# Kernel optimization log

Hardware: AMD Instinct MI355X
Metric: run time of the kernel (lower is better)

Reference implementation:

```python
import jax, jax.numpy as jnp
import numpy as np

N_NODES = 100000
NEG_SLOPE = 0.2  # PyG GATConv default LeakyReLU slope


def gat_conv(x, W, att_src, att_dst, bias, edge_index, num_nodes, concat):
    """PyG-style GATConv with default add_self_loops=True.
    x: [N, Fin], W: [Fin, H*C], att_src/att_dst: [H, C], bias: [H*C] or [C].
    """
    H, C = att_src.shape
    h = (x @ W).reshape(num_nodes, H, C)              # [N, H, C]
    # append self-loops (PyG default)
    loops = jnp.arange(num_nodes, dtype=edge_index.dtype)
    src = jnp.concatenate([edge_index[0], loops])     # [E+N]
    dst = jnp.concatenate([edge_index[1], loops])
    # per-node attention logits, then per-edge score
    a_src = jnp.sum(h * att_src[None], axis=-1)       # [N, H]
    a_dst = jnp.sum(h * att_dst[None], axis=-1)       # [N, H]
    e = jax.nn.leaky_relu(a_src[src] + a_dst[dst], NEG_SLOPE)  # [E+N, H]
    # softmax over incoming edges of each destination node
    m = jax.ops.segment_max(e, dst, num_segments=num_nodes)    # [N, H]
    e = jnp.exp(e - m[dst])
    denom = jax.ops.segment_sum(e, dst, num_segments=num_nodes)
    alpha = e / denom[dst]                                      # [E+N, H]
    # scatter-aggregate weighted source features
    msg = h[src] * alpha[..., None]                             # [E+N, H, C]
    out = jax.ops.segment_sum(msg, dst, num_segments=num_nodes)  # [N, H, C]
    if concat:
        out = out.reshape(num_nodes, H * C)
    else:
        out = out.mean(axis=1)
    return out + bias


def setup_inputs() -> dict:
    key = jax.random.key(0)
    ks = jax.random.split(key, 12)
    N, E = N_NODES, 1600000
    Fin, Ch, Hh, Cout = 128, 64, 2, 64

    def glorot(k, shape):
        fan = shape[0] + shape[-1]
        return jax.random.uniform(k, shape, jnp.float32, -1.0, 1.0) * np.sqrt(6.0 / fan)

    x = jax.random.normal(ks[0], (N, Fin), jnp.float32)
    edge_index = jax.random.randint(ks[1], (2, E), 0, N, jnp.int32)
    W1 = glorot(ks[2], (Fin, Hh * Ch))
    att_src1 = glorot(ks[3], (Hh, Ch))
    att_dst1 = glorot(ks[4], (Hh, Ch))
    b1 = jnp.zeros((Hh * Ch,), jnp.float32)
    W2 = glorot(ks[5], (Hh * Ch, Cout))
    att_src2 = glorot(ks[6], (1, Cout))
    att_dst2 = glorot(ks[7], (1, Cout))
    b2 = jnp.zeros((Cout,), jnp.float32)
    return {"x": x, "edge_index": edge_index,
            "W1": W1, "att_src1": att_src1, "att_dst1": att_dst1, "b1": b1,
            "W2": W2, "att_src2": att_src2, "att_dst2": att_dst2, "b2": b2}


def reference(x, edge_index, W1, att_src1, att_dst1, b1, W2, att_src2, att_dst2, b2):
    h = gat_conv(x, W1, att_src1, att_dst1, b1, edge_index, N_NODES, concat=True)
    h = jax.nn.elu(h)
    out = gat_conv(h, W2, att_src2, att_dst2, b2, edge_index, N_NODES, concat=True)
    return out
```

## Files before the change

kernel.cpp:

```cpp
#include <hip/hip_runtime.h>
#include <hip/hip_bf16.h>
#include <cstdint>
#include <cstddef>

static constexpr int FIN = 128;
static constexpr int HC1 = 128;
static constexpr int EPB = 4096;

typedef __attribute__((ext_vector_type(8))) short short8;
typedef __attribute__((ext_vector_type(4))) float f32x4;

__device__ __forceinline__ float bf2f(unsigned int u) { return __uint_as_float(u << 16); }
__device__ __forceinline__ unsigned short f2bf(float f) {
  unsigned int u = __float_as_uint(f);
  return (unsigned short)((u + 0x7fff + ((u >> 16) & 1)) >> 16);
}
__device__ __forceinline__ float lrelu02(float x) { return x > 0.f ? x : 0.2f * x; }
__device__ __forceinline__ int rl_i(int v, int l) { return __builtin_amdgcn_readlane(v, l); }
__device__ __forceinline__ unsigned int q8b(float x, float inv) {
  float q = fminf(fmaxf(x * inv, -127.f), 127.f);
  return (unsigned int)((int)rintf(q) + 128) & 255u;
}
#define NEG_INF __int_as_float(0xff800000)

__global__ __launch_bounds__(256) void bucket_hist(const int* __restrict__ dst,
                                                   int* __restrict__ bhist, int E, int NB) {
  __shared__ int lh[512];
  int t = threadIdx.x;
  lh[t] = 0; lh[t + 256] = 0;
  __syncthreads();
  int e0 = blockIdx.x * EPB;
  #pragma unroll
  for (int i = 0; i < EPB / 256; i++) {
    int e = e0 + i * 256 + t;
    if (e < E) atomicAdd(&lh[dst[e] >> 8], 1);
  }
  __syncthreads();
  for (int x = t; x < NB; x += 256) {
    int c = lh[x];
    if (c > 0) atomicAdd(&bhist[x], c);
  }
}

__global__ __launch_bounds__(512) void scan_buckets(const int* __restrict__ bhist,
                                                    int* __restrict__ boffs, int n) {
  __shared__ int sh[512];
  int t = threadIdx.x;
  int v = (t < n) ? bhist[t] : 0;
  sh[t] = v; __syncthreads();
  for (int d = 1; d < 512; d <<= 1) {
    int w = (t >= d) ? sh[t - d] : 0;
    __syncthreads();
    sh[t] += w;
    __syncthreads();
  }
  if (t <= n) boffs[t] = sh[t] - v;
}

__global__ __launch_bounds__(256) void bucket_scatter(const int* __restrict__ src,
                                                      const int* __restrict__ dst,
                                                      const int* __restrict__ boffs,
                                                      int* __restrict__ gcur,
                                                      unsigned int* __restrict__ sorted,
                                                      int E, int NB) {
  __shared__ int lh[512];
  int t = threadIdx.x;
  lh[t] = 0; lh[t + 256] = 0;
  __syncthreads();
  int e0 = blockIdx.x * EPB;
  #pragma unroll
  for (int i = 0; i < EPB / 256; i++) {
    int e = e0 + i * 256 + t;
    if (e < E) atomicAdd(&lh[dst[e] >> 8], 1);
  }
  __syncthreads();
  for (int x = t; x < NB; x += 256) {
    int c = lh[x];
    lh[x] = (c > 0) ? (boffs[x] + atomicAdd(&gcur[x], c)) : 0;
  }
  __syncthreads();
  #pragma unroll
  for (int i = 0; i < EPB / 256; i++) {
    int e = e0 + i * 256 + t;
    if (e < E) {
      int d = dst[e];
      int pos = atomicAdd(&lh[d >> 8], 1);
      sorted[pos] = ((unsigned int)src[e] << 8) | (unsigned int)(d & 255);
    }
  }
}

__global__ __launch_bounds__(256) void bucket_place_fused(const unsigned int* __restrict__ sorted,
                                                          const int* __restrict__ boffs,
                                                          int* __restrict__ offs,
                                                          int* __restrict__ ssrc,
                                                          int N, int E) {
  __shared__ int cnt[256];
  __shared__ int pref[256];
  int b = blockIdx.x, t = threadIdx.x;
  cnt[t] = 0;
  __syncthreads();
  int beg = boffs[b], end = boffs[b + 1];
  for (int p = beg + t; p < end; p += 256)
    atomicAdd(&cnt[sorted[p] & 255u], 1);
  __syncthreads();
  int v = cnt[t];
  pref[t] = v; __syncthreads();
  for (int d = 1; d < 256; d <<= 1) {
    int w = (t >= d) ? pref[t - d] : 0;
    __syncthreads();
    pref[t] += w;
    __syncthreads();
  }
  int excl = pref[t] - v;
  int node = b * 256 + t;
  if (node < N) offs[node] = beg + excl;
  if (b == 0 && t == 0) offs[N] = E;
  cnt[t] = beg + excl;
  __syncthreads();
  for (int p = beg + t; p < end; p += 256) {
    unsigned int pk = sorted[p];
    int dl = pk & 255u;
    int r = atomicAdd(&cnt[dl], 1);
    ssrc[r] = (int)(pk >> 8);
  }
}

template <int COLS, bool AF32>
__global__ __launch_bounds__(256) void gemm_mfma(const void* __restrict__ Av,
                                                 const float* __restrict__ Wv,
                                                 const float* __restrict__ att_s,
                                                 const float* __restrict__ att_d,
                                                 unsigned char* __restrict__ Cq,
                                                 float* __restrict__ scl,
                                                 float* __restrict__ asrc,
                                                 float* __restrict__ adst,
                                                 int nrows) {
  constexpr int NT = COLS / 16;
  constexpr int H = COLS / 64;
  __shared__ unsigned short WT[COLS][136];
  __shared__ __align__(16) unsigned char pack[4][16 * COLS];

  const int tid = threadIdx.x;
  constexpr int NPC = COLS / 4;
  for (int idx = tid; idx < 128 * NPC; idx += 256) {
    int k = idx / NPC;
    int n0 = (idx - k * NPC) * 4;
    float4 wv = *(const float4*)(Wv + (size_t)k * COLS + n0);
    WT[n0 + 0][k] = f2bf(wv.x);
    WT[n0 + 1][k] = f2bf(wv.y);
    WT[n0 + 2][k] = f2bf(wv.z);
    WT[n0 + 3][k] = f2bf(wv.w);
  }

  const int w = tid >> 6, lane = tid & 63;
  const int quad = lane >> 4, cl = lane & 15;
  const int rbase = blockIdx.x * 128 + w * 32;

  float asv[NT], adv[NT];
  #pragma unroll
  for (int ct = 0; ct < NT; ct++) {
    asv[ct] = att_s[ct * 16 + cl];
    adv[ct] = att_d[ct * 16 + cl];
  }
  __syncthreads();

  f32x4 acc[2][NT];
  #pragma unroll
  for (int rt = 0; rt < 2; rt++)
    #pragma unroll
    for (int ct = 0; ct < NT; ct++) acc[rt][ct] = (f32x4){0.f, 0.f, 0.f, 0.f};

  #pragma unroll
  for (int kc = 0; kc < 4; kc++) {
    const int k0 = kc * 32 + quad * 8;
    short8 a[2];
    #pragma unroll
    for (int rt = 0; rt < 2; rt++) {
      int row = rbase + rt * 16 + cl;
      row = min(row, nrows - 1);
      if constexpr (AF32) {
        const float* ap = (const float*)Av + (size_t)row * 128 + k0;
        float4 f0 = *(const float4*)ap;
        float4 f1 = *(const float4*)(ap + 4);
        short8 t;
        t[0] = (short)f2bf(f0.x); t[1] = (short)f2bf(f0.y);
        t[2] = (short)f2bf(f0.z); t[3] = (short)f2bf(f0.w);
        t[4] = (short)f2bf(f1.x); t[5] = (short)f2bf(f1.y);
        t[6] = (short)f2bf(f1.z); t[7] = (short)f2bf(f1.w);
        a[rt] = t;
      } else {
        a[rt] = *(const short8*)((const unsigned short*)Av + (size_t)row * 128 + k0);
      }
    }
    #pragma unroll
    for (int ct = 0; ct < NT; ct++) {
      short8 b = *(const short8*)&WT[ct * 16 + cl][k0];
      #pragma unroll
      for (int rt = 0; rt < 2; rt++)
        acc[rt][ct] = __builtin_amdgcn_mfma_f32_16x16x32_bf16(a[rt], b, acc[rt][ct], 0, 0, 0);
    }
  }

  #pragma unroll
  for (int rt = 0; rt < 2; rt++) {
    #pragma unroll
    for (int r = 0; r < 4; r++) {
      int grow = rbase + rt * 16 + quad * 4 + r;
      float s0 = 0.f, s1 = 0.f, d0 = 0.f, d1 = 0.f;
      float mx = 0.f;
      #pragma unroll
      for (int ct = 0; ct < NT; ct++) {
        float av = acc[rt][ct][r];
        mx = fmaxf(mx, fabsf(av));
        if (H == 2 && ct >= NT / 2) {
          s1 = fmaf(av, asv[ct], s1);
          d1 = fmaf(av, adv[ct], d1);
        } else {
          s0 = fmaf(av, asv[ct], s0);
          d0 = fmaf(av, adv[ct], d0);
        }
      }
      #pragma unroll
      for (int dd = 8; dd >= 1; dd >>= 1) {
        mx = fmaxf(mx, __shfl_xor(mx, dd));
        s0 += __shfl_xor(s0, dd);
        d0 += __shfl_xor(d0, dd);
        if (H == 2) {
          s1 += __shfl_xor(s1, dd);
          d1 += __shfl_xor(d1, dd);
        }
      }
      float inv = mx > 0.f ? 127.f / mx : 0.f;
      if (cl == 0 && grow < nrows) {
        scl[grow] = mx * (1.f / 127.f);
        if (H == 2) {
          ((float2*)asrc)[grow] = make_float2(s0, s1);
          ((float2*)adst)[grow] = make_float2(d0, d1);
        } else {
          asrc[grow] = s0;
          adst[grow] = d0;
        }
      }
      #pragma unroll
      for (int ct = 0; ct < NT; ct++)
        pack[w][(quad * 4 + r) * COLS + ct * 16 + cl] =
            (unsigned char)q8b(acc[rt][ct][r], inv);
    }
    __syncthreads();
    if constexpr (COLS == 128) {
      #pragma unroll
      for (int i = 0; i < 2; i++) {
        int off = i * 1024 + lane * 16;
        uint4 v = *(const uint4*)&pack[w][off];
        int grow = rbase + rt * 16 + (off >> 7);
        if (grow < nrows)
          *(uint4*)(Cq + (size_t)grow * 128 + (off & 127)) = v;
      }
    } else {
      int off = lane * 16;
      uint4 v = *(const uint4*)&pack[w][off];
      int grow = rbase + rt * 16 + (off >> 6);
      if (grow < nrows)
        *(uint4*)(Cq + (size_t)grow * 64 + (off & 63)) = v;
    }
    __syncthreads();
  }
}

template <int H, bool ELU_OUT, bool F32OUT>
__global__ __launch_bounds__(256) void agg_gather(const void* __restrict__ hq,
                                                  const float* __restrict__ scl,
                                                  const float* __restrict__ asrc,
                                                  const float* __restrict__ adst,
                                                  const int* __restrict__ offs,
                                                  const int* __restrict__ ssrc,
                                                  const float* __restrict__ bias,
                                                  void* __restrict__ outv, int n) {
  __shared__ float pshare[4][64];
  __shared__ int vshare[4][64];
  const int tid = threadIdx.x;
  const int wid = tid >> 6;
  int node = (int)((blockIdx.x * (unsigned)blockDim.x + tid) >> 6);
  int lane = tid & 63;
  if (node >= n) return;
  const int hd = lane >> 5;
  const int beg = offs[node], end = offs[node + 1];
  const unsigned short* hq16 = (const unsigned short*)hq;
  const unsigned char* hqb = (const unsigned char*)hq;

  float adh, m, acc0, acc1, d;
  float SPF = 0.f;
  const float s_self = scl[node];
  if constexpr (H == 2) {
    float2 adv = ((const float2*)adst)[node];
    float2 asv = ((const float2*)asrc)[node];
    adh = hd ? adv.y : adv.x;
    m = lrelu02((hd ? asv.y : asv.x) + adh);
    unsigned int v = hq16[((size_t)node << 6) + lane];
    acc0 = s_self * ((float)(v & 255u) - 128.f);
    acc1 = s_self * ((float)((v >> 8) & 255u) - 128.f);
  } else {
    adh = adst[node];
    m = lrelu02(asrc[node] + adh);
    if (hd == 0) {
      unsigned int v = hq16[((size_t)node << 5) + lane];
      acc0 = s_self * ((float)(v & 255u) - 128.f);
      acc1 = s_self * ((float)((v >> 8) & 255u) - 128.f);
    } else {
      acc0 = 0.f; acc1 = 0.f;
    }
  }
  d = 1.f;

  constexpr int CH = (H == 2) ? 32 : 64;
  const int lvoff = (lane & 31) * 2;
  for (int pos = beg; pos < end; pos += CH) {
    const int len = min(CH, end - pos);
    int li = (H == 2) ? (lane & 31) : lane;
    bool valid = li < len;
    int s_l = valid ? ssrc[pos + li] : 0;
    float scl_l = valid ? scl[s_l] : 0.f;
    float e_l;
    if constexpr (H == 2) {
      float a = asrc[(s_l << 1) + hd];
      e_l = valid ? lrelu02(a + adh) : NEG_INF;
    } else {
      float a = asrc[s_l];
      e_l = valid ? lrelu02(a + adh) : NEG_INF;
    }
    float mc = e_l;
    #pragma unroll
    for (int dlt = CH >> 1; dlt >= 1; dlt >>= 1) mc = fmaxf(mc, __shfl_xor(mc, dlt));
    float m_new = fmaxf(m, mc);
    float f = __expf(m - m_new);
    float p_l = __expf(e_l - m_new);
    float sc = p_l;
    #pragma unroll
    for (int dlt = CH >> 1; dlt >= 1; dlt >>= 1) sc += __shfl_xor(sc, dlt);
    d = d * f + sc;
    acc0 *= f; acc1 *= f;
    m = m_new;
    p_l *= scl_l;

    pshare[wid][lane] = p_l;
    float spf = p_l;
    if constexpr (H == 2) {
      #pragma unroll
      for (int dlt = 16; dlt >= 1; dlt >>= 1) spf += __shfl_xor(spf, dlt);
    } else {
      vshare[wid][lane] = s_l << 6;
      #pragma unroll
      for (int dlt = 32; dlt >= 1; dlt >>= 1) spf += __shfl_xor(spf, dlt);
    }
    SPF = SPF * f + spf;

    if constexpr (H == 2) {
      const int ng = (len + 7) >> 3;
      for (int g = 0; g < ng; g++) {
        const int jb = g * 8;
        unsigned short v[8];
        #pragma unroll
        for (int k = 0; k < 8; k++) {
          int s = rl_i(s_l, jb + k);
          v[k] = hq16[((size_t)(unsigned)s << 6) + lane];
        }
        float pv[8];
        #pragma unroll
        for (int k = 0; k < 8; k++) pv[k] = pshare[wid][hd * 32 + jb + k];
        #pragma unroll
        for (int k = 0; k < 8; k++) {
          unsigned int w = v[k];
          acc0 = fmaf(pv[k], (float)(w & 255u), acc0);
          acc1 = fmaf(pv[k], (float)((w >> 8) & 255u), acc1);
        }
      }
    } else {
      const int npair = (len + 1) >> 1;
      const int ng = (npair + 7) >> 3;
      for (int g = 0; g < ng; g++) {
        const int jb = g * 16;
        unsigned short v[8];
        #pragma unroll
        for (int k = 0; k < 8; k++) {
          int voff = vshare[wid][jb + 2 * k + hd];
          v[k] = *(const unsigned short*)(hqb + (unsigned)voff + lvoff);
        }
        float pv[8];
        #pragma unroll
        for (int k = 0; k < 8; k++) pv[k] = pshare[wid][jb + 2 * k + hd];
        #pragma unroll
        for (int k = 0; k < 8; k++) {
          unsigned int w = v[k];
          acc0 = fmaf(pv[k], (float)(w & 255u), acc0);
          acc1 = fmaf(pv[k], (float)((w >> 8) & 255u), acc1);
        }
      }
    }
  }

  if constexpr (H == 1) {
    acc0 += __shfl_xor(acc0, 32);
    acc1 += __shfl_xor(acc1, 32);
  }
  acc0 = fmaf(-128.f, SPF, acc0);
  acc1 = fmaf(-128.f, SPF, acc1);

  const float inv = 1.f / d;
  if constexpr (H == 2) {
    float2 bv = ((const float2*)bias)[lane];
    float v0 = acc0 * inv + bv.x;
    float v1 = acc1 * inv + bv.y;
    if (ELU_OUT) {
      v0 = v0 > 0.f ? v0 : (__expf(v0) - 1.f);
      v1 = v1 > 0.f ? v1 : (__expf(v1) - 1.f);
    }
    if constexpr (F32OUT) {
      ((float2*)outv)[(size_t)node * 64 + lane] = make_float2(v0, v1);
    } else {
      unsigned int pk = (unsigned int)f2bf(v0) | ((unsigned int)f2bf(v1) << 16);
      ((unsigned int*)outv)[(size_t)node * 64 + lane] = pk;
    }
  } else {
    if (hd == 0) {
      float2 bv = ((const float2*)bias)[lane];
      float v0 = acc0 * inv + bv.x;
      float v1 = acc1 * inv + bv.y;
      if (ELU_OUT) {
        v0 = v0 > 0.f ? v0 : (__expf(v0) - 1.f);
        v1 = v1 > 0.f ? v1 : (__expf(v1) - 1.f);
      }
      if constexpr (F32OUT) {
        ((float2*)outv)[(size_t)node * 32 + lane] = make_float2(v0, v1);
      } else {
        unsigned int pk = (unsigned int)f2bf(v0) | ((unsigned int)f2bf(v1) << 16);
        ((unsigned int*)outv)[(size_t)node * 32 + lane] = pk;
      }
    }
  }
}

extern "C" void kernel_launch(void* const* d_in, const int* in_sizes, int n_in,
                              void* d_out, int out_size, void* d_ws, size_t ws_size,
                              hipStream_t stream) {
  const int N = in_sizes[0] / FIN;
  const int E = in_sizes[1] / 2;

  const void*  x   = d_in[0];
  const int*   ei  = (const int*)d_in[1];
  const float* W1  = (const float*)d_in[2];
  const float* as1 = (const float*)d_in[3];
  const float* ad1 = (const float*)d_in[4];
  const float* b1  = (const float*)d_in[5];
  const float* W2  = (const float*)d_in[6];
  const float* as2 = (const float*)d_in[7];
  const float* ad2 = (const float*)d_in[8];
  const float* b2  = (const float*)d_in[9];

  const int* e_src = ei;
  const int* e_dst = ei + E;

  char* p = (char*)d_ws;
  auto carve = [&](size_t bytes) {
    char* q = p;
    p += (bytes + 255) & ~(size_t)255;
    return (void*)q;
  };
  unsigned char* h1q = (unsigned char*)carve((size_t)N * 128);
  float* scl1        = (float*)carve((size_t)N * 4);
  unsigned char* h2q = (unsigned char*)carve((size_t)N * 64);
  float* scl2        = (float*)carve((size_t)N * 4);
  unsigned short* buf2 = (unsigned short*)carve((size_t)N * HC1 * 2);
  float* asrc1 = (float*)carve((size_t)N * 2 * 4);
  float* adst1 = (float*)carve((size_t)N * 2 * 4);
  float* asrc2 = (float*)carve((size_t)N * 4);
  float* adst2 = (float*)carve((size_t)N * 4);
  int* offs    = (int*)carve((size_t)(N + 1) * 4);
  int* bhist   = (int*)carve((size_t)2 * 512 * 4);
  int* gcur    = bhist + 512;
  int* boffs   = (int*)carve(513 * 4);
  unsigned int* sorted = (unsigned int*)carve((size_t)E * 4);
  int* ssrc    = (int*)carve((size_t)E * 4);

  const int NB = (N + 255) >> 8;
  const int sgrid = (E + EPB - 1) / EPB;
  const int wgrid = (int)(((size_t)N * 64 + 255) / 256);
  const int ggrid = (N + 127) / 128;

  hipMemsetAsync(bhist, 0, (size_t)2 * 512 * 4, stream);
  bucket_hist<<<sgrid, 256, 0, stream>>>(e_dst, bhist, E, NB);
  scan_buckets<<<1, 512, 0, stream>>>(bhist, boffs, NB);
  bucket_scatter<<<sgrid, 256, 0, stream>>>(e_src, e_dst, boffs, gcur, sorted, E, NB);
  bucket_place_fused<<<NB, 256, 0, stream>>>(sorted, boffs, offs, ssrc, N, E);

  gemm_mfma<128, true><<<ggrid, 256, 0, stream>>>(x, W1, as1, ad1, h1q, scl1,
                                                  asrc1, adst1, N);
  agg_gather<2, true, false><<<wgrid, 256, 0, stream>>>(h1q, scl1, asrc1, adst1, offs, ssrc,
                                                        b1, buf2, N);

  gemm_mfma<64, false><<<ggrid, 256, 0, stream>>>(buf2, W2, as2, ad2, h2q, scl2,
                                                  asrc2, adst2, N);
  agg_gather<1, false, true><<<wgrid, 256, 0, stream>>>(h2q, scl2, asrc2, adst2, offs, ssrc,
                                                        b2, d_out, N);
}
```

Measured before the change: 311.1 us.

## Replace online softmax with global-max upper bound for attention normalization

The GEMM kernels now compute a global maximum of the source attention logits per head with atomicMax on order-preserving float keys. The aggregation kernel uses lrelu(max_src + a_dst) as a fixed per-node upper bound on the softmax shift. This removes the per-chunk wave max/sum reductions and the rescaling of accumulators from the online softmax, deferring the sums to one final reduction. The bound is valid because LeakyReLU is monotone, but a loose bound can cause exp underflow for nodes whose logits sit far below the global maximum.

```diff
diff --git a/kernel.cpp b/kernel.cpp
--- a/kernel.cpp
+++ b/kernel.cpp
@@ -20,6 +20,13 @@
 __device__ __forceinline__ unsigned int q8b(float x, float inv) {
   float q = fminf(fmaxf(x * inv, -127.f), 127.f);
   return (unsigned int)((int)rintf(q) + 128) & 255u;
+}
+__device__ __forceinline__ unsigned int fkey(float f) {
+  unsigned int u = __float_as_uint(f);
+  return (int)u < 0 ? ~u : (u | 0x80000000u);
+}
+__device__ __forceinline__ float fdec(unsigned int k) {
+  return __uint_as_float((int)k < 0 ? (k & 0x7fffffffu) : ~k);
 }
 #define NEG_INF __int_as_float(0xff800000)
 
@@ -135,6 +142,7 @@
                                                  float* __restrict__ scl,
                                                  float* __restrict__ asrc,
                                                  float* __restrict__ adst,
+                                                 unsigned int* __restrict__ gmax,
                                                  int nrows) {
   constexpr int NT = COLS / 16;
   constexpr int H = COLS / 64;
@@ -202,6 +210,7 @@
     }
   }
 
+  float lm0 = NEG_INF, lm1 = NEG_INF;
   #pragma unroll
   for (int rt = 0; rt < 2; rt++) {
     #pragma unroll
@@ -231,6 +240,8 @@
           d1 += __shfl_xor(d1, dd);
         }
       }
+      lm0 = fmaxf(lm0, s0);
+      if (H == 2) lm1 = fmaxf(lm1, s1);
       float inv = mx > 0.f ? 127.f / mx : 0.f;
       if (cl == 0 && grow < nrows) {
         scl[grow] = mx * (1.f / 127.f);
@@ -266,6 +277,17 @@
     }
     __syncthreads();
   }
+
+  lm0 = fmaxf(lm0, __shfl_xor(lm0, 16));
+  lm0 = fmaxf(lm0, __shfl_xor(lm0, 32));
+  if (H == 2) {
+    lm1 = fmaxf(lm1, __shfl_xor(lm1, 16));
+    lm1 = fmaxf(lm1, __shfl_xor(lm1, 32));
+  }
+  if (lane == 0) {
+    atomicMax(gmax + 0, fkey(lm0));
+    if (H == 2) atomicMax(gmax + 1, fkey(lm1));
+  }
 }
 
 template <int H, bool ELU_OUT, bool F32OUT>
@@ -273,6 +295,7 @@
                                                   const float* __restrict__ scl,
                                                   const float* __restrict__ asrc,
                                                   const float* __restrict__ adst,
+                                                  const unsigned int* __restrict__ gmax,
                                                   const int* __restrict__ offs,
                                                   const int* __restrict__ ssrc,
                                                   const float* __restrict__ bias,
@@ -289,29 +312,35 @@
   const unsigned short* hq16 = (const unsigned short*)hq;
   const unsigned char* hqb = (const unsigned char*)hq;
 
-  float adh, m, acc0, acc1, d;
-  float SPF = 0.f;
+  float adh, B, p_self, acc0, acc1;
   const float s_self = scl[node];
   if constexpr (H == 2) {
     float2 adv = ((const float2*)adst)[node];
     float2 asv = ((const float2*)asrc)[node];
     adh = hd ? adv.y : adv.x;
-    m = lrelu02((hd ? asv.y : asv.x) + adh);
+    float es = lrelu02((hd ? asv.y : asv.x) + adh);
+    B = lrelu02(fdec(gmax[hd]) + adh);
+    p_self = __expf(es - B);
     unsigned int v = hq16[((size_t)node << 6) + lane];
-    acc0 = s_self * ((float)(v & 255u) - 128.f);
-    acc1 = s_self * ((float)((v >> 8) & 255u) - 128.f);
+    float ps = p_self * s_self;
+    acc0 = ps * ((float)(v & 255u) - 128.f);
+    acc1 = ps * ((float)((v >> 8) & 255u) - 128.f);
   } else {
     adh = adst[node];
-    m = lrelu02(asrc[node] + adh);
+    float es = lrelu02(asrc[node] + adh);
+    B = lrelu02(fdec(gmax[0]) + adh);
+    p_self = __expf(es - B);
     if (hd == 0) {
       unsigned int v = hq16[((size_t)node << 5) + lane];
-      acc0 = s_self * ((float)(v & 255u) - 128.f);
-      acc1 = s_self * ((float)((v >> 8) & 255u) - 128.f);
+      float ps = p_self * s_self;
+      acc0 = ps * ((float)(v & 255u) - 128.f);
+      acc1 = ps * ((float)((v >> 8) & 255u) - 128.f);
     } else {
       acc0 = 0.f; acc1 = 0.f;
     }
   }
-  d = 1.f;
+  float dacc = 0.f;
+  float SPF = 0.f;
 
   constexpr int CH = (H == 2) ? 32 : 64;
   const int lvoff = (lane & 31) * 2;
@@ -321,39 +350,16 @@
     bool valid = li < len;
     int s_l = valid ? ssrc[pos + li] : 0;
     float scl_l = valid ? scl[s_l] : 0.f;
-    float e_l;
-    if constexpr (H == 2) {
-      float a = asrc[(s_l << 1) + hd];
-      e_l = valid ? lrelu02(a + adh) : NEG_INF;
-    } else {
-      float a = asrc[s_l];
-      e_l = valid ? lrelu02(a + adh) : NEG_INF;
-    }
-    float mc = e_l;
-    #pragma unroll
-    for (int dlt = CH >> 1; dlt >= 1; dlt >>= 1) mc = fmaxf(mc, __shfl_xor(mc, dlt));
-    float m_new = fmaxf(m, mc);
-    float f = __expf(m - m_new);
-    float p_l = __expf(e_l - m_new);
-    float sc = p_l;
-    #pragma unroll
-    for (int dlt = CH >> 1; dlt >= 1; dlt >>= 1) sc += __shfl_xor(sc, dlt);
-    d = d * f + sc;
-    acc0 *= f; acc1 *= f;
-    m = m_new;
+    float a;
+    if constexpr (H == 2) a = asrc[(s_l << 1) + hd];
+    else                  a = asrc[s_l];
+    float e_l = lrelu02(a + adh);
+    float p_l = valid ? __expf(e_l - B) : 0.f;
+    dacc += p_l;
     p_l *= scl_l;
-
+    SPF += p_l;
     pshare[wid][lane] = p_l;
-    float spf = p_l;
-    if constexpr (H == 2) {
-      #pragma unroll
-      for (int dlt = 16; dlt >= 1; dlt >>= 1) spf += __shfl_xor(spf, dlt);
-    } else {
-      vshare[wid][lane] = s_l << 6;
-      #pragma unroll
-      for (int dlt = 32; dlt >= 1; dlt >>= 1) spf += __shfl_xor(spf, dlt);
-    }
-    SPF = SPF * f + spf;
+    if constexpr (H == 1) vshare[wid][lane] = s_l << 6;
 
     if constexpr (H == 2) {
       const int ng = (len + 7) >> 3;
@@ -399,12 +405,24 @@
     }
   }
 
-  if constexpr (H == 1) {
+  if constexpr (H == 2) {
+    #pragma unroll
+    for (int dlt = 16; dlt >= 1; dlt >>= 1) {
+      dacc += __shfl_xor(dacc, dlt);
+      SPF  += __shfl_xor(SPF, dlt);
+    }
+  } else {
+    #pragma unroll
+    for (int dlt = 32; dlt >= 1; dlt >>= 1) {
+      dacc += __shfl_xor(dacc, dlt);
+      SPF  += __shfl_xor(SPF, dlt);
+    }
     acc0 += __shfl_xor(acc0, 32);
     acc1 += __shfl_xor(acc1, 32);
   }
   acc0 = fmaf(-128.f, SPF, acc0);
   acc1 = fmaf(-128.f, SPF, acc1);
+  const float d = p_self + dacc;
 
   const float inv = 1.f / d;
   if constexpr (H == 2) {
@@ -476,8 +494,9 @@
   float* asrc2 = (float*)carve((size_t)N * 4);
   float* adst2 = (float*)carve((size_t)N * 4);
   int* offs    = (int*)carve((size_t)(N + 1) * 4);
-  int* bhist   = (int*)carve((size_t)2 * 512 * 4);
+  int* bhist   = (int*)carve((size_t)(2 * 512 + 8) * 4);
   int* gcur    = bhist + 512;
+  unsigned int* gmax = (unsigned int*)(bhist + 1024);
   int* boffs   = (int*)carve(513 * 4);
   unsigned int* sorted = (unsigned int*)carve((size_t)E * 4);
   int* ssrc    = (int*)carve((size_t)E * 4);
@@ -487,19 +506,19 @@
   const int wgrid = (int)(((size_t)N * 64 + 255) / 256);
   const int ggrid = (N + 127) / 128;
 
-  hipMemsetAsync(bhist, 0, (size_t)2 * 512 * 4, stream);
+  hipMemsetAsync(bhist, 0, (size_t)(2 * 512 + 8) * 4, stream);
   bucket_hist<<<sgrid, 256, 0, stream>>>(e_dst, bhist, E, NB);
   scan_buckets<<<1, 512, 0, stream>>>(bhist, boffs, NB);
   bucket_scatter<<<sgrid, 256, 0, stream>>>(e_src, e_dst, boffs, gcur, sorted, E, NB);
   bucket_place_fused<<<NB, 256, 0, stream>>>(sorted, boffs, offs, ssrc, N, E);
 
   gemm_mfma<128, true><<<ggrid, 256, 0, stream>>>(x, W1, as1, ad1, h1q, scl1,
-                                                  asrc1, adst1, N);
-  agg_gather<2, true, false><<<wgrid, 256, 0, stream>>>(h1q, scl1, asrc1, adst1, offs, ssrc,
-                                                        b1, buf2, N);
+                                                  asrc1, adst1, gmax, N);
+  agg_gather<2, true, false><<<wgrid, 256, 0, stream>>>(h1q, scl1, asrc1, adst1, gmax,
+                                                        offs, ssrc, b1, buf2, N);
 
   gemm_mfma<64, false><<<ggrid, 256, 0, stream>>>(buf2, W2, as2, ad2, h2q, scl2,
-                                                  asrc2, adst2, N);
-  agg_gather<1, false, true><<<wgrid, 256, 0, stream>>>(h2q, scl2, asrc2, adst2, offs, ssrc,
-                                                        b2, d_out, N);
-}
+                                                  asrc2, adst2, gmax + 2, N);
+  agg_gather<1, false, true><<<wgrid, 256, 0, stream>>>(h2q, scl2, asrc2, adst2, gmax + 2,
+                                                        offs, ssrc, b2, d_out, N);
+}
```

Measured after the change: 407.7 us. 31.1% more time.
